# Optimization experiments

Hardware: AMD Instinct MI355X
Metric: run time of the kernel (lower is better)

## Reference

```python
import jax, jax.numpy as jnp
import numpy as np

B, N, H = 64, 1024, 64
ALPHA = 0.2  # leaky relu negative slope
NEG_BIG = -1.0e12


def setup_inputs() -> dict:
    key = jax.random.key(0)
    k1, k2, k3, k4, k5, k6 = jax.random.split(key, 6)
    inp = jax.random.normal(k1, (B, N, H), dtype=jnp.float32)
    inp_none = jax.random.normal(k2, (B, N, H), dtype=jnp.float32)
    A = (jax.random.uniform(k3, (B, N, N)) < 0.1).astype(jnp.float32)
    # per-sample [i, j] ranges, i <= j < N
    l = jnp.sort(jax.random.randint(k4, (B, 2), 0, N), axis=1)
    # xavier_uniform with gain=1.414 on shape (2H, 1)
    bound = 1.414 * np.sqrt(6.0 / (2 * H + 1))
    a_i = jax.random.uniform(k5, (2 * H, 1), minval=-bound, maxval=bound, dtype=jnp.float32)
    a_c = jax.random.uniform(k6, (2 * H, 1), minval=-bound, maxval=bound, dtype=jnp.float32)
    return {"inp": inp, "inp_none": inp_none, "A": A, "l": l, "a_i": a_i, "a_c": a_c}


def reference(inp, inp_none, A, l, a_i, a_c):
    h = inp.shape[-1]
    n = inp.shape[1]
    # additive-score halves: [B, N, 1]
    Wh1_i = inp_none @ a_i[:h]
    Wh2_i = inp @ a_i[h:]
    Wh1_c = inp @ a_c[:h]
    Wh2_c = inp @ a_c[h:]
    # vectorized replacement of the per-sample range overwrite loop:
    # rows in [l[b,0], l[b,1]) take the a_i branch
    pos = jnp.arange(n)[None, :, None]                       # [1, N, 1]
    in_range = (pos >= l[:, 0, None, None]) & (pos < l[:, 1, None, None])  # [B, N, 1]
    Wh1 = jnp.where(in_range, Wh1_i, Wh1_c)                  # [B, N, 1]
    Wh2 = jnp.where(in_range, Wh2_i, Wh2_c)                  # [B, N, 1]
    # e[b, p, q] = leakyrelu((Wh1[b,p] + Wh2[b,q]) * A[b,p,q])
    e = (Wh1 + jnp.swapaxes(Wh2, 1, 2)) * A                  # [B, N, N]
    e = jnp.where(e >= 0, e, ALPHA * e)
    attn = jnp.where(A > 0, e, NEG_BIG)
    attn = jax.nn.softmax(attn, axis=2)
    h_prime = attn @ inp                                     # [B, N, H]
    return jax.nn.elu(h_prime)  # concat=True
```

## Files before the change

kernel.cpp:

```cpp
#include <hip/hip_runtime.h>
#include <hip/hip_bf16.h>
#include <math.h>
#include <stdint.h>

constexpr int Bn = 64, Nn = 1024, Hn = 64;
constexpr float LRELU_ALPHA = 0.2f;

typedef __attribute__((ext_vector_type(8))) short bf16x8;
typedef __attribute__((ext_vector_type(4))) float f32x4;

__device__ __forceinline__ float lrelu(float x) { return x >= 0.f ? x : LRELU_ALPHA * x; }
__device__ __forceinline__ ushort f2bf(float x) {
    uint u = __float_as_uint(x);
    return (ushort)((u + 0x7FFFu + ((u >> 16) & 1u)) >> 16);
}
__device__ __forceinline__ float bf2f(ushort b) { return __uint_as_float(((uint)b) << 16); }

__global__ __launch_bounds__(256) void wh_kernel(
    const float* __restrict__ inp, const float* __restrict__ inp_none,
    const int* __restrict__ l, const float* __restrict__ a_i,
    const float* __restrict__ a_c,
    float* __restrict__ Wh1, float* __restrict__ Wh2)
{
    const int wave = threadIdx.x >> 6;
    const int lane = threadIdx.x & 63;
    const int row  = blockIdx.x * 4 + wave;
    const int b    = row >> 10;
    const int n    = row & (Nn - 1);

    const int l0 = l[b * 2], l1 = l[b * 2 + 1];
    const bool in_range = (n >= l0) && (n < l1);

    const size_t base = (size_t)row * Hn + lane;
    const float x1  = in_range ? inp_none[base] : inp[base];
    const float x2  = inp[base];
    const float av1 = in_range ? a_i[lane]      : a_c[lane];
    const float av2 = in_range ? a_i[Hn + lane] : a_c[Hn + lane];

    float p1 = x1 * av1;
    float p2 = x2 * av2;
    #pragma unroll
    for (int off = 32; off > 0; off >>= 1) {
        p1 += __shfl_xor(p1, off);
        p2 += __shfl_xor(p2, off);
    }
    if (lane == 0) {
        Wh1[row] = p1;
        Wh2[row] = p2;
    }
}

__global__ __launch_bounds__(256) void tconv_kernel(const float* __restrict__ inp,
                                                    ushort* __restrict__ inpT)
{
    __shared__ ushort tile[64][74];
    const int b  = blockIdx.x >> 4;
    const int q0 = (blockIdx.x & 15) << 6;
    const int t  = threadIdx.x;
    {
        const int q  = t >> 2;
        const int h0 = (t & 3) << 4;
        const float* src = inp + ((size_t)(b * Nn + q0 + q) * Hn + h0);
        uint* dst = (uint*)&tile[q][h0];
        #pragma unroll
        for (int i = 0; i < 4; ++i) {
            const float4 v = *(const float4*)(src + 4 * i);
            dst[2 * i + 0] = (uint)f2bf(v.x) | ((uint)f2bf(v.y) << 16);
            dst[2 * i + 1] = (uint)f2bf(v.z) | ((uint)f2bf(v.w) << 16);
        }
    }
    __syncthreads();
    {
        const int h  = t >> 2;
        const int qb = (t & 3) << 4;
        uint w[8];
        #pragma unroll
        for (int i = 0; i < 8; ++i)
            w[i] = (uint)tile[qb + 2 * i][h] | ((uint)tile[qb + 2 * i + 1][h] << 16);
        uint4* dst = (uint4*)(inpT + ((size_t)(b * Hn + h) * Nn + q0 + qb));
        dst[0] = make_uint4(w[0], w[1], w[2], w[3]);
        dst[1] = make_uint4(w[4], w[5], w[6], w[7]);
    }
}

__global__ __launch_bounds__(256, 4) void gat_mfma_kernel(
    const float* __restrict__ A, const ushort* __restrict__ inpT,
    const float* __restrict__ Wh1, const float* __restrict__ Wh2,
    float* __restrict__ out)
{
    __shared__ __align__(16) char pool[18560];
    float* wh2_lds = (float*)(pool + 16384);
    float* rs_part = (float*)(pool + 17408);
    float* inv_lds = (float*)(pool + 18432);
    float* out_lds = (float*)pool;

    const int t    = threadIdx.x;
    const int wave = t >> 6;
    const int lane = t & 63;

    const int d = blockIdx.x;
    const int o = (d & 7) * 256 + (d >> 3);
    const int b  = o >> 5;
    const int p0 = (o & 31) << 5;

    const float*  Ab   = A + (size_t)b * Nn * Nn;
    const float*  Wh2b = Wh2 + b * Nn;
    const ushort* Tb   = inpT + (size_t)b * Hn * Nn;

    const int r  = t >> 3;
    const int qo = (t & 7) << 2;
    const float wh1_r = Wh1[b * Nn + p0 + r];
    const float* Arow = Ab + (size_t)(p0 + r) * Nn;

    const int l15 = lane & 15;
    const int lg  = lane >> 4;
    const ushort* a_src = Tb + (size_t)(wave * 16 + l15) * Nn + lg * 8;
    const uint bswz = ((uint)(l15 & 7)) << 4;
    const uint row0 = (uint)(l15 * 512);
    const uint row1 = (uint)((l15 + 16) * 512);

    f32x4 acc0 = {0.f, 0.f, 0.f, 0.f};
    f32x4 acc1 = {0.f, 0.f, 0.f, 0.f};
    float rs_local = 0.f;

    for (int c = 0; c < 4; ++c) {
        const int q0 = c * 256;
        wh2_lds[t] = Wh2b[q0 + t];
        __syncthreads();

        #pragma unroll
        for (int j = 0; j < 8; ++j) {
            const int q = qo + 32 * j;
            const float4 a4 = *(const float4*)(Arow + q0 + q);
            const float4 w2 = *(const float4*)(wh2_lds + q);
            const float s0 = lrelu(wh1_r + w2.x);
            const float s1 = lrelu(wh1_r + w2.y);
            const float s2 = lrelu(wh1_r + w2.z);
            const float s3 = lrelu(wh1_r + w2.w);
            const ushort u0 = f2bf(a4.x > 0.f ? __expf(s0) : 0.f);
            const ushort u1 = f2bf(a4.y > 0.f ? __expf(s1) : 0.f);
            const ushort u2 = f2bf(a4.z > 0.f ? __expf(s2) : 0.f);
            const ushort u3 = f2bf(a4.w > 0.f ? __expf(s3) : 0.f);
            rs_local += (bf2f(u0) + bf2f(u1)) + (bf2f(u2) + bf2f(u3));
            const uint lo = (uint)u0 | ((uint)u1 << 16);
            const uint hi = (uint)u2 | ((uint)u3 << 16);
            const uint byte = ((uint)(r * 512 + q * 2)) ^ (((uint)(r & 7)) << 4);
            *(uint2*)(pool + byte) = make_uint2(lo, hi);
        }
        __syncthreads();

        #pragma unroll
        for (int kk = 0; kk < 8; ++kk) {
            const uint col = ((uint)(lg * 16 + kk * 64)) ^ bswz;
            const bf16x8 af = *(const bf16x8*)(a_src + q0 + kk * 32);
            const bf16x8 b0 = *(const bf16x8*)(pool + (row0 + col));
            const bf16x8 b1 = *(const bf16x8*)(pool + (row1 + col));
            acc0 = __builtin_amdgcn_mfma_f32_16x16x32_bf16(af, b0, acc0, 0, 0, 0);
            acc1 = __builtin_amdgcn_mfma_f32_16x16x32_bf16(af, b1, acc1, 0, 0, 0);
        }
        __syncthreads();
    }

    rs_part[t] = rs_local;
    __syncthreads();
    if (t < 32) {
        float s = 0.f;
        #pragma unroll
        for (int j = 0; j < 8; ++j) s += rs_part[t * 8 + j];
        inv_lds[t] = s > 0.f ? 1.f / s : 0.f;
    }
    __syncthreads();

    #pragma unroll
    for (int nt = 0; nt < 2; ++nt) {
        const int p = nt * 16 + l15;
        const float inv = inv_lds[p];
        const f32x4 a = nt ? acc1 : acc0;
        #pragma unroll
        for (int rg = 0; rg < 4; ++rg) {
            const int h = wave * 16 + lg * 4 + rg;
            out_lds[p * 65 + h] = a[rg] * inv;
        }
    }
    __syncthreads();

    {
        const int p  = t >> 3;
        const int h0 = (t & 7) << 3;
        float v[8];
        #pragma unroll
        for (int i = 0; i < 8; ++i) {
            const float x = out_lds[p * 65 + h0 + i];
            v[i] = x > 0.f ? x : expm1f(x);
        }
        float* orow = out + (size_t)(b * Nn + p0 + p) * Hn + h0;
        *(float4*)(orow)     = make_float4(v[0], v[1], v[2], v[3]);
        *(float4*)(orow + 4) = make_float4(v[4], v[5], v[6], v[7]);
    }
}

__global__ __launch_bounds__(256) void gat_fallback_kernel(
    const float* __restrict__ inp, const float* __restrict__ A,
    const float* __restrict__ Wh1, const float* __restrict__ Wh2,
    float* __restrict__ out)
{
    __shared__ float wlds[4][256];
    __shared__ int   qlds[4][256];
    const int wave = threadIdx.x >> 6;
    const int lane = threadIdx.x & 63;
    const int cpx = gridDim.x >> 3;
    const int bid = blockIdx.x;
    const int swz = (bid & 7) * cpx + (bid >> 3);
    const int row = swz * 4 + wave;
    const int b   = row >> 10;
    const int p   = row & (Nn - 1);
    const float* Arow = A + ((size_t)b * Nn + p) * Nn;
    const float* Wh2b = Wh2 + b * Nn;
    const float  wh1p = Wh1[b * Nn + p];
    float4 sv[4];
    float  m = -INFINITY;
    #pragma unroll
    for (int k = 0; k < 4; ++k) {
        const int q0 = k * 256 + lane * 4;
        const float4 a4 = *(const float4*)(Arow + q0);
        const float4 w2 = *(const float4*)(Wh2b + q0);
        float4 s;
        s.x = (a4.x > 0.f) ? lrelu(wh1p + w2.x) : -INFINITY;
        s.y = (a4.y > 0.f) ? lrelu(wh1p + w2.y) : -INFINITY;
        s.z = (a4.z > 0.f) ? lrelu(wh1p + w2.z) : -INFINITY;
        s.w = (a4.w > 0.f) ? lrelu(wh1p + w2.w) : -INFINITY;
        sv[k] = s;
        m = fmaxf(m, fmaxf(fmaxf(s.x, s.y), fmaxf(s.z, s.w)));
    }
    #pragma unroll
    for (int off = 32; off > 0; off >>= 1) m = fmaxf(m, __shfl_xor(m, off));
    const bool empty = (m == -INFINITY);
    const float* inpb = inp + (size_t)b * Nn * Hn;
    float acc0 = 0.f, acc1 = 0.f;
    if (!empty) {
        float4 wv[4];
        float  lsum = 0.f;
        #pragma unroll
        for (int k = 0; k < 4; ++k) {
            float4 s = sv[k];
            float4 w;
            w.x = __expf(s.x - m); w.y = __expf(s.y - m);
            w.z = __expf(s.z - m); w.w = __expf(s.w - m);
            wv[k] = w;
            lsum += (w.x + w.y) + (w.z + w.w);
        }
        #pragma unroll
        for (int off = 32; off > 0; off >>= 1) lsum += __shfl_xor(lsum, off);
        const float inv = 1.f / lsum;
        int c = 0;
        #pragma unroll
        for (int k = 0; k < 4; ++k)
            #pragma unroll
            for (int cc = 0; cc < 4; ++cc)
                c += (((const float*)&wv[k])[cc] != 0.f) ? 1 : 0;
        int s = c;
        #pragma unroll
        for (int off = 1; off < 64; off <<= 1) {
            const int tt = __shfl_up(s, off);
            if (lane >= off) s += tt;
        }
        int j   = s - c;
        int cnt = __shfl(s, 63);
        #pragma unroll
        for (int k = 0; k < 4; ++k)
            #pragma unroll
            for (int cc = 0; cc < 4; ++cc) {
                const float w = ((const float*)&wv[k])[cc];
                if (w != 0.f && j < 256) {
                    wlds[wave][j] = w;
                    qlds[wave][j] = (k * 256 + lane * 4 + cc) * Hn;
                    ++j;
                }
            }
        if (cnt > 256) cnt = 256;
        asm volatile("s_waitcnt lgkmcnt(0)" ::: "memory");
        int i = 0;
        for (; i + 4 <= cnt; i += 4) {
            const float w0 = wlds[wave][i], w1 = wlds[wave][i + 1];
            const float w2 = wlds[wave][i + 2], w3 = wlds[wave][i + 3];
            const int o0 = qlds[wave][i], o1 = qlds[wave][i + 1];
            const int o2 = qlds[wave][i + 2], o3 = qlds[wave][i + 3];
            acc0 = fmaf(w0, inpb[o0 + lane], acc0);
            acc1 = fmaf(w1, inpb[o1 + lane], acc1);
            acc0 = fmaf(w2, inpb[o2 + lane], acc0);
            acc1 = fmaf(w3, inpb[o3 + lane], acc1);
        }
        for (; i < cnt; ++i)
            acc0 = fmaf(wlds[wave][i], inpb[qlds[wave][i] + lane], acc0);
        acc0 = (acc0 + acc1) * inv;
    } else {
        for (int q = 0; q < Nn; ++q) acc0 += inpb[q * Hn + lane];
        acc0 *= (1.f / Nn);
    }
    const float rr = acc0 > 0.f ? acc0 : expm1f(acc0);
    out[(size_t)row * Hn + lane] = rr;
}

extern "C" void kernel_launch(void* const* d_in, const int* in_sizes, int n_in,
                              void* d_out, int out_size, void* d_ws, size_t ws_size,
                              hipStream_t stream) {
    const float* inp      = (const float*)d_in[0];
    const float* inp_none = (const float*)d_in[1];
    const float* A        = (const float*)d_in[2];
    const int*   l        = (const int*)d_in[3];
    const float* a_i      = (const float*)d_in[4];
    const float* a_c      = (const float*)d_in[5];
    float* out = (float*)d_out;

    float*  Wh1  = (float*)d_ws;
    float*  Wh2  = Wh1 + Bn * Nn;
    ushort* inpT = (ushort*)((char*)d_ws + (size_t)2 * Bn * Nn * 4);

    const size_t need = (size_t)2 * Bn * Nn * 4 + (size_t)Bn * Hn * Nn * 2;

    wh_kernel<<<Bn * Nn / 4, 256, 0, stream>>>(inp, inp_none, l, a_i, a_c, Wh1, Wh2);

    if (ws_size >= need) {
        tconv_kernel<<<Bn * 16, 256, 0, stream>>>(inp, inpT);
        gat_mfma_kernel<<<Bn * 32, 256, 0, stream>>>(A, inpT, Wh1, Wh2, out);
    } else {
        gat_fallback_kernel<<<Bn * Nn / 4, 256, 0, stream>>>(inp, A, Wh1, Wh2, out);
    }
}
```

Baseline: 425.7 us.

## Fuse Wh projection into transpose prep and prefetch A rows in registers

Merges the Wh1/Wh2 projection into the bf16 transpose kernel, removing one launch and a second pass over inp. In the main kernel, all of Wh2 is staged in LDS once, and the next 256-column chunk of A is prefetched into registers while the current chunk's MFMAs run. It also raises the launch-bounds occupancy hint from 4 to 6 and swaps __syncthreads for a lighter LDS-only barrier. The costs are higher register pressure from the prefetch buffer and more LDS per block.

```diff
diff --git a/kernel.cpp b/kernel.cpp
--- a/kernel.cpp
+++ b/kernel.cpp
@@ -15,6 +15,207 @@
     return (ushort)((u + 0x7FFFu + ((u >> 16) & 1u)) >> 16);
 }
 __device__ __forceinline__ float bf2f(ushort b) { return __uint_as_float(((uint)b) << 16); }
+
+#define LDS_BARRIER()                                             \
+    do {                                                          \
+        asm volatile("s_waitcnt lgkmcnt(0)" ::: "memory");        \
+        __builtin_amdgcn_s_barrier();                             \
+        asm volatile("" ::: "memory");                            \
+    } while (0)
+
+__global__ __launch_bounds__(256) void prep_kernel(
+    const float* __restrict__ inp, const float* __restrict__ inp_none,
+    const int* __restrict__ l, const float* __restrict__ a_i,
+    const float* __restrict__ a_c,
+    ushort* __restrict__ inpT, float* __restrict__ Wh1, float* __restrict__ Wh2)
+{
+    __shared__ ushort tile[64][74];
+    const int b  = blockIdx.x >> 4;
+    const int q0 = (blockIdx.x & 15) << 6;
+    const int t  = threadIdx.x;
+    const int l0 = l[b * 2], l1 = l[b * 2 + 1];
+
+    {
+        const int q    = t >> 2;
+        const int h0   = (t & 3) << 4;
+        const int grow = q0 + q;
+        const bool in_range = (grow >= l0) && (grow < l1);
+
+        const float* src  = inp + ((size_t)(b * Nn + grow) * Hn + h0);
+        const float* av2p = (in_range ? a_i : a_c) + Hn + h0;
+        uint* dst = (uint*)&tile[q][h0];
+
+        float p1 = 0.f, p2 = 0.f;
+        #pragma unroll
+        for (int i = 0; i < 4; ++i) {
+            const float4 v = *(const float4*)(src + 4 * i);
+            dst[2 * i + 0] = (uint)f2bf(v.x) | ((uint)f2bf(v.y) << 16);
+            dst[2 * i + 1] = (uint)f2bf(v.z) | ((uint)f2bf(v.w) << 16);
+            const float4 a2 = *(const float4*)(av2p + 4 * i);
+            p2 += (v.x * a2.x + v.y * a2.y) + (v.z * a2.z + v.w * a2.w);
+        }
+        if (in_range) {
+            const float* s1 = inp_none + ((size_t)(b * Nn + grow) * Hn + h0);
+            #pragma unroll
+            for (int i = 0; i < 4; ++i) {
+                const float4 v1 = *(const float4*)(s1 + 4 * i);
+                const float4 a1 = *(const float4*)(a_i + h0 + 4 * i);
+                p1 += (v1.x * a1.x + v1.y * a1.y) + (v1.z * a1.z + v1.w * a1.w);
+            }
+        } else {
+            const float* s1 = inp + ((size_t)(b * Nn + grow) * Hn + h0);
+            #pragma unroll
+            for (int i = 0; i < 4; ++i) {
+                const float4 v1 = *(const float4*)(s1 + 4 * i);
+                const float4 a1 = *(const float4*)(a_c + h0 + 4 * i);
+                p1 += (v1.x * a1.x + v1.y * a1.y) + (v1.z * a1.z + v1.w * a1.w);
+            }
+        }
+        p1 += __shfl_xor(p1, 1); p1 += __shfl_xor(p1, 2);
+        p2 += __shfl_xor(p2, 1); p2 += __shfl_xor(p2, 2);
+        if ((t & 3) == 0) {
+            Wh1[b * Nn + grow] = p1;
+            Wh2[b * Nn + grow] = p2;
+        }
+    }
+    __syncthreads();
+    {
+        const int h  = t >> 2;
+        const int qb = (t & 3) << 4;
+        uint w[8];
+        #pragma unroll
+        for (int i = 0; i < 8; ++i)
+            w[i] = (uint)tile[qb + 2 * i][h] | ((uint)tile[qb + 2 * i + 1][h] << 16);
+        uint4* dst = (uint4*)(inpT + ((size_t)(b * Hn + h) * Nn + q0 + qb));
+        dst[0] = make_uint4(w[0], w[1], w[2], w[3]);
+        dst[1] = make_uint4(w[4], w[5], w[6], w[7]);
+    }
+}
+
+__global__ __launch_bounds__(256, 6) void gat_mfma_kernel(
+    const float* __restrict__ A, const ushort* __restrict__ inpT,
+    const float* __restrict__ Wh1, const float* __restrict__ Wh2,
+    float* __restrict__ out)
+{
+    __shared__ __align__(16) char pool[21632];
+    float* wh2_lds = (float*)(pool + 16384);
+    float* rs_part = (float*)(pool + 20480);
+    float* inv_lds = (float*)(pool + 21504);
+    float* out_lds = (float*)pool;
+
+    const int t    = threadIdx.x;
+    const int wave = t >> 6;
+    const int lane = t & 63;
+
+    const int d = blockIdx.x;
+    const int o = (d & 7) * 256 + (d >> 3);
+    const int b  = o >> 5;
+    const int p0 = (o & 31) << 5;
+
+    const float*  Ab   = A + (size_t)b * Nn * Nn;
+    const float*  Wh2b = Wh2 + b * Nn;
+    const ushort* Tb   = inpT + (size_t)b * Hn * Nn;
+
+    const int r  = t >> 3;
+    const int qo = (t & 7) << 2;
+    const float wh1_r = Wh1[b * Nn + p0 + r];
+    const float* Arow = Ab + (size_t)(p0 + r) * Nn;
+
+    const int l15 = lane & 15;
+    const int lg  = lane >> 4;
+    const ushort* a_src = Tb + (size_t)(wave * 16 + l15) * Nn + lg * 8;
+    const uint bswz = ((uint)(l15 & 7)) << 4;
+    const uint row0 = (uint)(l15 * 512);
+    const uint row1 = (uint)((l15 + 16) * 512);
+
+    float4 aReg[8];
+    #pragma unroll
+    for (int j = 0; j < 8; ++j) aReg[j] = *(const float4*)(Arow + qo + 32 * j);
+    #pragma unroll
+    for (int w = 0; w < 4; ++w) wh2_lds[w * 256 + t] = Wh2b[w * 256 + t];
+    LDS_BARRIER();
+
+    f32x4 acc0 = {0.f, 0.f, 0.f, 0.f};
+    f32x4 acc1 = {0.f, 0.f, 0.f, 0.f};
+    float rs_local = 0.f;
+
+    #pragma unroll
+    for (int c = 0; c < 4; ++c) {
+        #pragma unroll
+        for (int j = 0; j < 8; ++j) {
+            const int qq = qo + 32 * j;
+            const float4 a4 = aReg[j];
+            const float4 w2 = *(const float4*)(wh2_lds + c * 256 + qq);
+            const float s0 = lrelu(wh1_r + w2.x);
+            const float s1 = lrelu(wh1_r + w2.y);
+            const float s2 = lrelu(wh1_r + w2.z);
+            const float s3 = lrelu(wh1_r + w2.w);
+            const ushort u0 = f2bf(a4.x > 0.f ? __expf(s0) : 0.f);
+            const ushort u1 = f2bf(a4.y > 0.f ? __expf(s1) : 0.f);
+            const ushort u2 = f2bf(a4.z > 0.f ? __expf(s2) : 0.f);
+            const ushort u3 = f2bf(a4.w > 0.f ? __expf(s3) : 0.f);
+            rs_local += (bf2f(u0) + bf2f(u1)) + (bf2f(u2) + bf2f(u3));
+            const uint lo = (uint)u0 | ((uint)u1 << 16);
+            const uint hi = (uint)u2 | ((uint)u3 << 16);
+            const uint byte = ((uint)(r * 512 + qq * 2)) ^ (((uint)(r & 7)) << 4);
+            *(uint2*)(pool + byte) = make_uint2(lo, hi);
+        }
+        if (c < 3) {
+            #pragma unroll
+            for (int j = 0; j < 8; ++j)
+                aReg[j] = *(const float4*)(Arow + (c + 1) * 256 + qo + 32 * j);
+        }
+        LDS_BARRIER();
+
+        #pragma unroll
+        for (int kk = 0; kk < 8; ++kk) {
+            const uint col = ((uint)(lg * 16 + kk * 64)) ^ bswz;
+            const bf16x8 af = *(const bf16x8*)(a_src + c * 256 + kk * 32);
+            const bf16x8 b0 = *(const bf16x8*)(pool + (row0 + col));
+            const bf16x8 b1 = *(const bf16x8*)(pool + (row1 + col));
+            acc0 = __builtin_amdgcn_mfma_f32_16x16x32_bf16(af, b0, acc0, 0, 0, 0);
+            acc1 = __builtin_amdgcn_mfma_f32_16x16x32_bf16(af, b1, acc1, 0, 0, 0);
+        }
+        LDS_BARRIER();
+    }
+
+    rs_part[t] = rs_local;
+    __syncthreads();
+    if (t < 32) {
+        float s = 0.f;
+        #pragma unroll
+        for (int j = 0; j < 8; ++j) s += rs_part[t * 8 + j];
+        inv_lds[t] = s > 0.f ? 1.f / s : 0.f;
+    }
+    __syncthreads();
+
+    #pragma unroll
+    for (int nt = 0; nt < 2; ++nt) {
+        const int p = nt * 16 + l15;
+        const float inv = inv_lds[p];
+        const f32x4 a = nt ? acc1 : acc0;
+        #pragma unroll
+        for (int rg = 0; rg < 4; ++rg) {
+            const int h = wave * 16 + lg * 4 + rg;
+            out_lds[p * 65 + h] = a[rg] * inv;
+        }
+    }
+    __syncthreads();
+
+    {
+        const int p  = t >> 3;
+        const int h0 = (t & 7) << 3;
+        float v[8];
+        #pragma unroll
+        for (int i = 0; i < 8; ++i) {
+            const float x = out_lds[p * 65 + h0 + i];
+            v[i] = x > 0.f ? x : expm1f(x);
+        }
+        float* orow = out + (size_t)(b * Nn + p0 + p) * Hn + h0;
+        *(float4*)(orow)     = make_float4(v[0], v[1], v[2], v[3]);
+        *(float4*)(orow + 4) = make_float4(v[4], v[5], v[6], v[7]);
+    }
+}
 
 __global__ __launch_bounds__(256) void wh_kernel(
     const float* __restrict__ inp, const float* __restrict__ inp_none,
@@ -27,16 +228,13 @@
     const int row  = blockIdx.x * 4 + wave;
     const int b    = row >> 10;
     const int n    = row & (Nn - 1);
-
     const int l0 = l[b * 2], l1 = l[b * 2 + 1];
     const bool in_range = (n >= l0) && (n < l1);
-
     const size_t base = (size_t)row * Hn + lane;
     const float x1  = in_range ? inp_none[base] : inp[base];
     const float x2  = inp[base];
     const float av1 = in_range ? a_i[lane]      : a_c[lane];
     const float av2 = in_range ? a_i[Hn + lane] : a_c[Hn + lane];
-
     float p1 = x1 * av1;
     float p2 = x2 * av2;
     #pragma unroll
@@ -44,159 +242,7 @@
         p1 += __shfl_xor(p1, off);
         p2 += __shfl_xor(p2, off);
     }
-    if (lane == 0) {
-        Wh1[row] = p1;
-        Wh2[row] = p2;
-    }
-}
-
-__global__ __launch_bounds__(256) void tconv_kernel(const float* __restrict__ inp,
-                                                    ushort* __restrict__ inpT)
-{
-    __shared__ ushort tile[64][74];
-    const int b  = blockIdx.x >> 4;
-    const int q0 = (blockIdx.x & 15) << 6;
-    const int t  = threadIdx.x;
-    {
-        const int q  = t >> 2;
-        const int h0 = (t & 3) << 4;
-        const float* src = inp + ((size_t)(b * Nn + q0 + q) * Hn + h0);
-        uint* dst = (uint*)&tile[q][h0];
-        #pragma unroll
-        for (int i = 0; i < 4; ++i) {
-            const float4 v = *(const float4*)(src + 4 * i);
-            dst[2 * i + 0] = (uint)f2bf(v.x) | ((uint)f2bf(v.y) << 16);
-            dst[2 * i + 1] = (uint)f2bf(v.z) | ((uint)f2bf(v.w) << 16);
-        }
-    }
-    __syncthreads();
-    {
-        const int h  = t >> 2;
-        const int qb = (t & 3) << 4;
-        uint w[8];
-        #pragma unroll
-        for (int i = 0; i < 8; ++i)
-            w[i] = (uint)tile[qb + 2 * i][h] | ((uint)tile[qb + 2 * i + 1][h] << 16);
-        uint4* dst = (uint4*)(inpT + ((size_t)(b * Hn + h) * Nn + q0 + qb));
-        dst[0] = make_uint4(w[0], w[1], w[2], w[3]);
-        dst[1] = make_uint4(w[4], w[5], w[6], w[7]);
-    }
-}
-
-__global__ __launch_bounds__(256, 4) void gat_mfma_kernel(
-    const float* __restrict__ A, const ushort* __restrict__ inpT,
-    const float* __restrict__ Wh1, const float* __restrict__ Wh2,
-    float* __restrict__ out)
-{
-    __shared__ __align__(16) char pool[18560];
-    float* wh2_lds = (float*)(pool + 16384);
-    float* rs_part = (float*)(pool + 17408);
-    float* inv_lds = (float*)(pool + 18432);
-    float* out_lds = (float*)pool;
-
-    const int t    = threadIdx.x;
-    const int wave = t >> 6;
-    const int lane = t & 63;
-
-    const int d = blockIdx.x;
-    const int o = (d & 7) * 256 + (d >> 3);
-    const int b  = o >> 5;
-    const int p0 = (o & 31) << 5;
-
-    const float*  Ab   = A + (size_t)b * Nn * Nn;
-    const float*  Wh2b = Wh2 + b * Nn;
-    const ushort* Tb   = inpT + (size_t)b * Hn * Nn;
-
-    const int r  = t >> 3;
-    const int qo = (t & 7) << 2;
-    const float wh1_r = Wh1[b * Nn + p0 + r];
-    const float* Arow = Ab + (size_t)(p0 + r) * Nn;
-
-    const int l15 = lane & 15;
-    const int lg  = lane >> 4;
-    const ushort* a_src = Tb + (size_t)(wave * 16 + l15) * Nn + lg * 8;
-    const uint bswz = ((uint)(l15 & 7)) << 4;
-    const uint row0 = (uint)(l15 * 512);
-    const uint row1 = (uint)((l15 + 16) * 512);
-
-    f32x4 acc0 = {0.f, 0.f, 0.f, 0.f};
-    f32x4 acc1 = {0.f, 0.f, 0.f, 0.f};
-    float rs_local = 0.f;
-
-    for (int c = 0; c < 4; ++c) {
-        const int q0 = c * 256;
-        wh2_lds[t] = Wh2b[q0 + t];
-        __syncthreads();
-
-        #pragma unroll
-        for (int j = 0; j < 8; ++j) {
-            const int q = qo + 32 * j;
-            const float4 a4 = *(const float4*)(Arow + q0 + q);
-            const float4 w2 = *(const float4*)(wh2_lds + q);
-            const float s0 = lrelu(wh1_r + w2.x);
-            const float s1 = lrelu(wh1_r + w2.y);
-            const float s2 = lrelu(wh1_r + w2.z);
-            const float s3 = lrelu(wh1_r + w2.w);
-            const ushort u0 = f2bf(a4.x > 0.f ? __expf(s0) : 0.f);
-            const ushort u1 = f2bf(a4.y > 0.f ? __expf(s1) : 0.f);
-            const ushort u2 = f2bf(a4.z > 0.f ? __expf(s2) : 0.f);
-            const ushort u3 = f2bf(a4.w > 0.f ? __expf(s3) : 0.f);
-            rs_local += (bf2f(u0) + bf2f(u1)) + (bf2f(u2) + bf2f(u3));
-            const uint lo = (uint)u0 | ((uint)u1 << 16);
-            const uint hi = (uint)u2 | ((uint)u3 << 16);
-            const uint byte = ((uint)(r * 512 + q * 2)) ^ (((uint)(r & 7)) << 4);
-            *(uint2*)(pool + byte) = make_uint2(lo, hi);
-        }
-        __syncthreads();
-
-        #pragma unroll
-        for (int kk = 0; kk < 8; ++kk) {
-            const uint col = ((uint)(lg * 16 + kk * 64)) ^ bswz;
-            const bf16x8 af = *(const bf16x8*)(a_src + q0 + kk * 32);
-            const bf16x8 b0 = *(const bf16x8*)(pool + (row0 + col));
-            const bf16x8 b1 = *(const bf16x8*)(pool + (row1 + col));
-            acc0 = __builtin_amdgcn_mfma_f32_16x16x32_bf16(af, b0, acc0, 0, 0, 0);
-            acc1 = __builtin_amdgcn_mfma_f32_16x16x32_bf16(af, b1, acc1, 0, 0, 0);
-        }
-        __syncthreads();
-    }
-
-    rs_part[t] = rs_local;
-    __syncthreads();
-    if (t < 32) {
-        float s = 0.f;
-        #pragma unroll
-        for (int j = 0; j < 8; ++j) s += rs_part[t * 8 + j];
-        inv_lds[t] = s > 0.f ? 1.f / s : 0.f;
-    }
-    __syncthreads();
-
-    #pragma unroll
-    for (int nt = 0; nt < 2; ++nt) {
-        const int p = nt * 16 + l15;
-        const float inv = inv_lds[p];
-        const f32x4 a = nt ? acc1 : acc0;
-        #pragma unroll
-        for (int rg = 0; rg < 4; ++rg) {
-            const int h = wave * 16 + lg * 4 + rg;
-            out_lds[p * 65 + h] = a[rg] * inv;
-        }
-    }
-    __syncthreads();
-
-    {
-        const int p  = t >> 3;
-        const int h0 = (t & 7) << 3;
-        float v[8];
-        #pragma unroll
-        for (int i = 0; i < 8; ++i) {
-            const float x = out_lds[p * 65 + h0 + i];
-            v[i] = x > 0.f ? x : expm1f(x);
-        }
-        float* orow = out + (size_t)(b * Nn + p0 + p) * Hn + h0;
-        *(float4*)(orow)     = make_float4(v[0], v[1], v[2], v[3]);
-        *(float4*)(orow + 4) = make_float4(v[4], v[5], v[6], v[7]);
-    }
+    if (lane == 0) { Wh1[row] = p1; Wh2[row] = p2; }
 }
 
 __global__ __launch_bounds__(256) void gat_fallback_kernel(
@@ -318,12 +364,12 @@
 
     const size_t need = (size_t)2 * Bn * Nn * 4 + (size_t)Bn * Hn * Nn * 2;
 
-    wh_kernel<<<Bn * Nn / 4, 256, 0, stream>>>(inp, inp_none, l, a_i, a_c, Wh1, Wh2);
-
     if (ws_size >= need) {
-        tconv_kernel<<<Bn * 16, 256, 0, stream>>>(inp, inpT);
+        prep_kernel<<<Bn * 16, 256, 0, stream>>>(inp, inp_none, l, a_i, a_c,
+                                                 inpT, Wh1, Wh2);
         gat_mfma_kernel<<<Bn * 32, 256, 0, stream>>>(A, inpT, Wh1, Wh2, out);
     } else {
+        wh_kernel<<<Bn * Nn / 4, 256, 0, stream>>>(inp, inp_none, l, a_i, a_c, Wh1, Wh2);
         gat_fallback_kernel<<<Bn * Nn / 4, 256, 0, stream>>>(inp, A, Wh1, Wh2, out);
     }
 }
```

Result: no change. 417.7 us (-1.9%).
